# Performance work log

Measured on AMD Instinct MI355X. Metric: run time of the kernel, lower is better.

Reference implementation:

```python
import jax, jax.numpy as jnp
import numpy as np

N = 50000   # num nodes
D = 64      # feature dim
E = 800000  # num edges (avg degree 16)


def setup_inputs() -> dict:
    key = jax.random.key(0)
    k1, k2, k3 = jax.random.split(key, 3)
    x = jax.random.normal(k1, (N, D), dtype=jnp.float32)
    edge_index = jax.random.randint(k2, (2, E), 0, N, dtype=jnp.int32)
    edge_weight = jax.random.uniform(k3, (E,), dtype=jnp.float32)
    return {"x": x, "edge_index": edge_index, "edge_weight": edge_weight}


def reference(x, edge_index, edge_weight):
    """Faithful translation of scatter_median (spmm with reduce='median'):
    per destination node, the (lower) median over its weighted incoming
    neighbor messages, computed independently per feature channel.
    Nodes with zero in-degree produce zeros (as in the torch code where
    h is initialized to zeros and degree-0 rows are skipped).
    """
    n, d = x.shape
    e = edge_index.shape[1]

    # sort edges by destination (stable sort; within-segment order is irrelevant for median)
    order = jnp.argsort(edge_index[1])
    row = edge_index[0, order]
    col = edge_index[1, order]
    w = edge_weight[order]

    # weighted messages: x_j = x[row] * w  -> [E, D]
    x_j = x[row] * w[:, None]

    # per-destination degree and position of each edge within its segment
    deg = jnp.bincount(col, length=n)                                   # [N]
    starts = jnp.concatenate([jnp.zeros(1, deg.dtype), jnp.cumsum(deg)[:-1]])
    pos = jnp.arange(e, dtype=deg.dtype) - starts[col]                  # [E]

    # dense batch [N, max_deg, D], padded with +inf so pads sort to the end
    max_deg = int(jnp.max(deg))  # concrete on materialized inputs
    dense = jnp.full((n, max_deg, d), jnp.inf, dtype=x.dtype)
    dense = dense.at[col, pos].set(x_j)

    # per-channel sort, then pick the lower-median index (torch.median semantics:
    # for even counts it returns the lower of the two middle values)
    dense = jnp.sort(dense, axis=1)
    idx = jnp.maximum((deg - 1) // 2, 0)                                # [N]
    med = jnp.take_along_axis(dense, idx[:, None, None], axis=1)[:, 0]  # [N, D]

    return jnp.where(deg[:, None] > 0, med, jnp.zeros((), dtype=x.dtype))
```

## Files before the change

kernel.cpp:

```cpp
#include <hip/hip_runtime.h>
#include <stdint.h>
#include <math.h>

#define NN 50000
#define DD 64
#define EE 800000
#define CAP 64

__global__ void zero_deg(int* __restrict__ deg) {
    int i = blockIdx.x * blockDim.x + threadIdx.x;
    if (i < NN) deg[i] = 0;
}

__global__ __launch_bounds__(256) void scatter_edges(
        const int* __restrict__ ei, const float* __restrict__ ew,
        int* __restrict__ deg, uint64_t* __restrict__ slots) {
    int t = blockIdx.x * blockDim.x + threadIdx.x;
    int e0 = t * 2;
    if (e0 >= EE) return;

    int2   src2 = *reinterpret_cast<const int2*>(ei + e0);
    int2   dst2 = *reinterpret_cast<const int2*>(ei + EE + e0);
    float2 w2   = *reinterpret_cast<const float2*>(ew + e0);

    int p0 = atomicAdd(&deg[dst2.x], 1);
    int p1 = atomicAdd(&deg[dst2.y], 1);

    if (p0 < CAP) {
        uint64_t wb = (uint64_t)__float_as_uint(w2.x);
        slots[(size_t)dst2.x * CAP + p0] = (wb << 32) | (uint32_t)src2.x;
    }
    if (p1 < CAP) {
        uint64_t wb = (uint64_t)__float_as_uint(w2.y);
        slots[(size_t)dst2.y * CAP + p1] = (wb << 32) | (uint32_t)src2.y;
    }
}

__device__ __forceinline__ void cswap(float& a, float& b) {
    float lo = fminf(a, b);
    float hi = fmaxf(a, b);
    a = lo; b = hi;
}

template<int I, int END, int R, int STEP, int PW>
struct Pairs {
    static __device__ __forceinline__ void run(float (&r)[PW]) {
        if constexpr (I + R < END) {
            cswap(r[I], r[I + R]);
            Pairs<I + STEP, END, R, STEP, PW>::run(r);
        }
    }
};

template<int LO, int N, int R, int PW>
struct Merge {
    static __device__ __forceinline__ void run(float (&r)[PW]) {
        if constexpr (2 * R < N) {
            Merge<LO,     N, 2 * R, PW>::run(r);
            Merge<LO + R, N, 2 * R, PW>::run(r);
            Pairs<LO + R, LO + N, R, 2 * R, PW>::run(r);
        } else {
            cswap(r[LO], r[LO + R]);
        }
    }
};

template<int LO, int N, int PW>
struct Sorter {
    static __device__ __forceinline__ void run(float (&r)[PW]) {
        if constexpr (N > 1) {
            Sorter<LO,         N / 2, PW>::run(r);
            Sorter<LO + N / 2, N / 2, PW>::run(r);
            Merge<LO, N, 1, PW>::run(r);
        }
    }
};

template <int PW>
__device__ __forceinline__ float gather_sort(const float* __restrict__ x, int lane,
                                             int dg, int k, int src_l, float w_l) {
    float r[PW];
    #pragma unroll
    for (int j = 0; j < PW; ++j) {
        int   sj = __builtin_amdgcn_readlane(src_l, j);
        float wj = __uint_as_float((uint32_t)__builtin_amdgcn_readlane(
                       (int)__float_as_uint(w_l), j));
        float v = INFINITY;
        if (j < dg)
            v = x[(size_t)(uint32_t)sj * DD + lane] * wj;
        r[j] = v;
    }
    Sorter<0, PW, PW>::run(r);
    constexpr int KLO = PW / 4;
    constexpr int KHI = (PW / 2 > 0) ? PW / 2 - 1 : 0;
    float med = r[KLO];
    #pragma unroll
    for (int t = KLO + 1; t <= KHI; ++t)
        if (t == k) med = r[t];
    return med;
}

__global__ __launch_bounds__(256, 4) void median_kernel(
    const float* __restrict__ x, const int* __restrict__ deg,
    const uint64_t* __restrict__ slots, float* __restrict__ out) {
    const int lane = threadIdx.x & 63;
    const int n = blockIdx.x * 4 + (threadIdx.x >> 6);
    if (n >= NN) return;

    int dg = deg[n];
    if (dg > CAP) dg = CAP;
    if (dg == 0) { out[(size_t)n * DD + lane] = 0.f; return; }

    uint64_t s = 0;
    if (lane < dg) s = slots[(size_t)n * CAP + lane];
    int   src_l = (int)(uint32_t)(s & 0xffffffffu);
    float w_l   = __uint_as_float((uint32_t)(s >> 32));

    const int k = (dg - 1) >> 1;
    float med;

    if      (dg <= 2)  med = gather_sort<2>(x, lane, dg, k, src_l, w_l);
    else if (dg <= 4)  med = gather_sort<4>(x, lane, dg, k, src_l, w_l);
    else if (dg <= 8)  med = gather_sort<8>(x, lane, dg, k, src_l, w_l);
    else if (dg <= 16) med = gather_sort<16>(x, lane, dg, k, src_l, w_l);
    else if (dg <= 32) med = gather_sort<32>(x, lane, dg, k, src_l, w_l);
    else               med = gather_sort<64>(x, lane, dg, k, src_l, w_l);

    out[(size_t)n * DD + lane] = med;
}

extern "C" void kernel_launch(void* const* d_in, const int* in_sizes, int n_in,
                              void* d_out, int out_size, void* d_ws, size_t ws_size,
                              hipStream_t stream) {
    const float*  x  = (const float*)d_in[0];
    const int*    ei = (const int*)d_in[1];
    const float*  ew = (const float*)d_in[2];
    float* out = (float*)d_out;

    int*      deg   = (int*)d_ws;
    uint64_t* slots = (uint64_t*)((char*)d_ws + (1 << 18));

    zero_deg<<<(NN + 255) / 256, 256, 0, stream>>>(deg);
    scatter_edges<<<(EE / 2 + 255) / 256, 256, 0, stream>>>(ei, ew, deg, slots);
    median_kernel<<<(NN + 3) / 4, 256, 0, stream>>>(x, deg, slots, out);
}
```

Before: 162.3 us.

## Partition per-node degree counters by XCD to localize scatter atomics

Replaces the single global per-destination atomic counter with eight per-XCD counter arrays, each owning six slots per node. A shared overflow counter supplies sixteen extra slots per node. The change aims to keep most atomics local to one XCD's L2 by using workgroup-scope atomics on per-XCD arrays, avoiding cross-die coherence traffic. The median kernel compacts the scattered slots with a ballot/popcount prefix search and shuffles before the gather and sort. This adds more counter zeroing and reads, and relies on the XCC_ID register, workgroup-scope atomics being safe across workgroups on the same XCD, and degree per node staying within 64, with overflow capped at 16.

```diff
diff --git a/kernel.cpp b/kernel.cpp
--- a/kernel.cpp
+++ b/kernel.cpp
@@ -5,34 +5,48 @@
 #define NN 50000
 #define DD 64
 #define EE 800000
-#define CAP 64
+#define NXCD 8
+#define PCAP 6
+#define OCAP 16
 
-__global__ void zero_deg(int* __restrict__ deg) {
+
+__global__ void zero_cnt(int* __restrict__ cnt) {
     int i = blockIdx.x * blockDim.x + threadIdx.x;
-    if (i < NN) deg[i] = 0;
+    if (i < NN * (NXCD + 1)) cnt[i] = 0;
 }
 
 __global__ __launch_bounds__(256) void scatter_edges(
         const int* __restrict__ ei, const float* __restrict__ ew,
-        int* __restrict__ deg, uint64_t* __restrict__ slots) {
+        int* __restrict__ deg8, int* __restrict__ ovf,
+        uint64_t* __restrict__ slots) {
     int t = blockIdx.x * blockDim.x + threadIdx.x;
     int e0 = t * 2;
     if (e0 >= EE) return;
+
+    unsigned xcd;
+    asm volatile("s_getreg_b32 %0, hwreg(HW_REG_XCC_ID)" : "=s"(xcd));
+    xcd &= (NXCD - 1);
 
     int2   src2 = *reinterpret_cast<const int2*>(ei + e0);
     int2   dst2 = *reinterpret_cast<const int2*>(ei + EE + e0);
     float2 w2   = *reinterpret_cast<const float2*>(ew + e0);
 
-    int p0 = atomicAdd(&deg[dst2.x], 1);
-    int p1 = atomicAdd(&deg[dst2.y], 1);
+    int   d[2] = {dst2.x, dst2.y};
+    int   s[2] = {src2.x, src2.y};
+    float w[2] = {w2.x, w2.y};
 
-    if (p0 < CAP) {
-        uint64_t wb = (uint64_t)__float_as_uint(w2.x);
-        slots[(size_t)dst2.x * CAP + p0] = (wb << 32) | (uint32_t)src2.x;
-    }
-    if (p1 < CAP) {
-        uint64_t wb = (uint64_t)__float_as_uint(w2.y);
-        slots[(size_t)dst2.y * CAP + p1] = (wb << 32) | (uint32_t)src2.y;
+    #pragma unroll
+    for (int i = 0; i < 2; ++i) {
+        uint64_t pk = ((uint64_t)__float_as_uint(w[i]) << 32) | (uint32_t)s[i];
+        size_t base = (size_t)d[i] * 64;
+        int p = __hip_atomic_fetch_add(&deg8[xcd * NN + d[i]], 1,
+                                       __ATOMIC_RELAXED, __HIP_MEMORY_SCOPE_WORKGROUP);
+        if (p < PCAP) {
+            slots[base + xcd * PCAP + p] = pk;
+        } else {
+            int q = atomicAdd(&ovf[d[i]], 1);
+            if (q < OCAP) slots[base + 48 + q] = pk;
+        }
     }
 }
 
@@ -101,20 +115,42 @@
 }
 
 __global__ __launch_bounds__(256, 4) void median_kernel(
-    const float* __restrict__ x, const int* __restrict__ deg,
-    const uint64_t* __restrict__ slots, float* __restrict__ out) {
+    const float* __restrict__ x, const int* __restrict__ deg8,
+    const int* __restrict__ ovf, const uint64_t* __restrict__ slots,
+    float* __restrict__ out) {
     const int lane = threadIdx.x & 63;
     const int n = blockIdx.x * 4 + (threadIdx.x >> 6);
     if (n >= NN) return;
 
-    int dg = deg[n];
-    if (dg > CAP) dg = CAP;
+    int cnt, pos;
+    if (lane < 48) {
+        int xc = lane / 6;
+        pos = lane - xc * 6;
+        cnt = deg8[xc * NN + n];
+        if (cnt > PCAP) cnt = PCAP;
+    } else {
+        pos = lane - 48;
+        cnt = ovf[n];
+        if (cnt > OCAP) cnt = OCAP;
+    }
+    uint64_t mask = __ballot(pos < cnt);
+    int dg = __popcll(mask);
+
     if (dg == 0) { out[(size_t)n * DD + lane] = 0.f; return; }
 
-    uint64_t s = 0;
-    if (lane < dg) s = slots[(size_t)n * CAP + lane];
-    int   src_l = (int)(uint32_t)(s & 0xffffffffu);
-    float w_l   = __uint_as_float((uint32_t)(s >> 32));
+    uint64_t s = slots[(size_t)n * 64 + lane];
+    int   src_raw = (int)(uint32_t)(s & 0xffffffffu);
+    float w_raw   = __uint_as_float((uint32_t)(s >> 32));
+
+    int idx = 0;
+    #pragma unroll
+    for (int step = 32; step >= 1; step >>= 1) {
+        int t2 = idx + step;
+        uint64_t lowmask = (t2 >= 64) ? ~0ull : ((1ull << t2) - 1ull);
+        if (__popcll(mask & lowmask) <= lane) idx = t2;
+    }
+    int   src_l = __shfl(src_raw, idx);
+    float w_l   = __shfl(w_raw, idx);
 
     const int k = (dg - 1) >> 1;
     float med;
@@ -137,10 +173,11 @@
     const float*  ew = (const float*)d_in[2];
     float* out = (float*)d_out;
 
-    int*      deg   = (int*)d_ws;
-    uint64_t* slots = (uint64_t*)((char*)d_ws + (1 << 18));
+    int*      deg8  = (int*)d_ws;
+    int*      ovf   = (int*)((char*)d_ws + (size_t)NXCD * NN * 4);
+    uint64_t* slots = (uint64_t*)((char*)d_ws + (1u << 21));
 
-    zero_deg<<<(NN + 255) / 256, 256, 0, stream>>>(deg);
-    scatter_edges<<<(EE / 2 + 255) / 256, 256, 0, stream>>>(ei, ew, deg, slots);
-    median_kernel<<<(NN + 3) / 4, 256, 0, stream>>>(x, deg, slots, out);
+    zero_cnt<<<(NN * (NXCD + 1) + 255) / 256, 256, 0, stream>>>(deg8);
+    scatter_edges<<<(EE / 2 + 255) / 256, 256, 0, stream>>>(ei, ew, deg8, ovf, slots);
+    median_kernel<<<(NN + 3) / 4, 256, 0, stream>>>(x, deg8, ovf, slots, out);
 }
```

Result: slower. 175.4 us (+8.1%).

## Bucketize edges by 64-node groups with shared-memory histograms before median

Applied to the files above, without the earlier changes.

Replaces per-edge global atomics into per-node slots with a two-level bucketing scheme. Each block builds a shared-memory histogram over 64-node buckets and reserves space with one global atomic per bucket, then writes packed records. The median kernel loads one bucket per block and scatters its records into per-node slots in LDS using shared atomics. The aim is to cut global atomic contention and scattered writes. Buckets are capped at 1536 records, so an unusually dense bucket would drop edges, and the median kernel now launches only 782 blocks that each process 64 nodes serially per wave.

```diff
diff --git a/kernel.cpp b/kernel.cpp
--- a/kernel.cpp
+++ b/kernel.cpp
@@ -5,34 +5,52 @@
 #define NN 50000
 #define DD 64
 #define EE 800000
-#define CAP 64
+#define BSZ 64
+#define NB 782
+#define BCAP 1536
+#define EPW 4096
 
-__global__ void zero_deg(int* __restrict__ deg) {
+
+__global__ void zero_cnt(int* __restrict__ cnt) {
     int i = blockIdx.x * blockDim.x + threadIdx.x;
-    if (i < NN) deg[i] = 0;
+    if (i < NB) cnt[i] = 0;
 }
 
-__global__ __launch_bounds__(256) void scatter_edges(
+__global__ __launch_bounds__(256) void bucketize(
         const int* __restrict__ ei, const float* __restrict__ ew,
-        int* __restrict__ deg, uint64_t* __restrict__ slots) {
-    int t = blockIdx.x * blockDim.x + threadIdx.x;
-    int e0 = t * 2;
-    if (e0 >= EE) return;
+        int* __restrict__ bucket_cnt, uint64_t* __restrict__ recs) {
+    __shared__ int hist[NB];
+    __shared__ int base[NB];
+    const int t = threadIdx.x;
+    const int e0 = blockIdx.x * EPW;
+    const int eend = (e0 + EPW < EE) ? e0 + EPW : EE;
 
-    int2   src2 = *reinterpret_cast<const int2*>(ei + e0);
-    int2   dst2 = *reinterpret_cast<const int2*>(ei + EE + e0);
-    float2 w2   = *reinterpret_cast<const float2*>(ew + e0);
+    for (int i = t; i < NB; i += 256) hist[i] = 0;
+    __syncthreads();
 
-    int p0 = atomicAdd(&deg[dst2.x], 1);
-    int p1 = atomicAdd(&deg[dst2.y], 1);
+    for (int e = e0 + t; e < eend; e += 256) {
+        int dst = ei[EE + e];
+        atomicAdd(&hist[dst >> 6], 1);
+    }
+    __syncthreads();
 
-    if (p0 < CAP) {
-        uint64_t wb = (uint64_t)__float_as_uint(w2.x);
-        slots[(size_t)dst2.x * CAP + p0] = (wb << 32) | (uint32_t)src2.x;
+    for (int i = t; i < NB; i += 256) {
+        int c = hist[i];
+        base[i] = (c > 0) ? atomicAdd(&bucket_cnt[i], c) : 0;
+        hist[i] = 0;
     }
-    if (p1 < CAP) {
-        uint64_t wb = (uint64_t)__float_as_uint(w2.y);
-        slots[(size_t)dst2.y * CAP + p1] = (wb << 32) | (uint32_t)src2.y;
+    __syncthreads();
+
+    for (int e = e0 + t; e < eend; e += 256) {
+        int   src = ei[e];
+        int   dst = ei[EE + e];
+        float w   = ew[e];
+        int   b   = dst >> 6;
+        int   p   = base[b] + atomicAdd(&hist[b], 1);
+        if (p < BCAP)
+            recs[(size_t)b * BCAP + p] =
+                ((uint64_t)__float_as_uint(w) << 32) |
+                ((uint32_t)src << 6) | (uint32_t)(dst & 63);
     }
 }
 
@@ -100,33 +118,56 @@
     return med;
 }
 
-__global__ __launch_bounds__(256, 4) void median_kernel(
-    const float* __restrict__ x, const int* __restrict__ deg,
-    const uint64_t* __restrict__ slots, float* __restrict__ out) {
-    const int lane = threadIdx.x & 63;
-    const int n = blockIdx.x * 4 + (threadIdx.x >> 6);
-    if (n >= NN) return;
+__global__ __launch_bounds__(256) void median_kernel(
+    const float* __restrict__ x, const int* __restrict__ bucket_cnt,
+    const uint64_t* __restrict__ recs, float* __restrict__ out) {
+    __shared__ uint64_t slot[BSZ * 64];
+    __shared__ int degl[BSZ];
+    const int t = threadIdx.x;
+    const int b = blockIdx.x;
 
-    int dg = deg[n];
-    if (dg > CAP) dg = CAP;
-    if (dg == 0) { out[(size_t)n * DD + lane] = 0.f; return; }
+    int cnt = bucket_cnt[b];
+    if (cnt > BCAP) cnt = BCAP;
 
-    uint64_t s = 0;
-    if (lane < dg) s = slots[(size_t)n * CAP + lane];
-    int   src_l = (int)(uint32_t)(s & 0xffffffffu);
-    float w_l   = __uint_as_float((uint32_t)(s >> 32));
+    for (int i = t; i < BSZ; i += 256) degl[i] = 0;
+    __syncthreads();
 
-    const int k = (dg - 1) >> 1;
-    float med;
+    const uint64_t* brec = recs + (size_t)b * BCAP;
+    for (int i = t; i < cnt; i += 256) {
+        uint64_t r = brec[i];
+        int loc = (int)(r & 63u);
+        int p = atomicAdd(&degl[loc], 1);
+        if (p < 64)
+            slot[loc * 64 + p] = (r & 0xFFFFFFFF00000000ull)
+                               | (uint32_t)(((uint32_t)r) >> 6);
+    }
+    __syncthreads();
 
-    if      (dg <= 2)  med = gather_sort<2>(x, lane, dg, k, src_l, w_l);
-    else if (dg <= 4)  med = gather_sort<4>(x, lane, dg, k, src_l, w_l);
-    else if (dg <= 8)  med = gather_sort<8>(x, lane, dg, k, src_l, w_l);
-    else if (dg <= 16) med = gather_sort<16>(x, lane, dg, k, src_l, w_l);
-    else if (dg <= 32) med = gather_sort<32>(x, lane, dg, k, src_l, w_l);
-    else               med = gather_sort<64>(x, lane, dg, k, src_l, w_l);
+    const int lane = t & 63;
+    const int wv   = t >> 6;
+    for (int loc = wv; loc < BSZ; loc += 4) {
+        int n = b * BSZ + loc;
+        if (n >= NN) break;
 
-    out[(size_t)n * DD + lane] = med;
+        int dg = __builtin_amdgcn_readfirstlane(degl[loc]);
+        if (dg > 64) dg = 64;
+
+        float med = 0.f;
+        if (dg > 0) {
+            uint64_t s = slot[loc * 64 + lane];
+            int   src_l = (int)(uint32_t)(s & 0xffffffffu);
+            float w_l   = __uint_as_float((uint32_t)(s >> 32));
+            const int k = (dg - 1) >> 1;
+
+            if      (dg <= 2)  med = gather_sort<2>(x, lane, dg, k, src_l, w_l);
+            else if (dg <= 4)  med = gather_sort<4>(x, lane, dg, k, src_l, w_l);
+            else if (dg <= 8)  med = gather_sort<8>(x, lane, dg, k, src_l, w_l);
+            else if (dg <= 16) med = gather_sort<16>(x, lane, dg, k, src_l, w_l);
+            else if (dg <= 32) med = gather_sort<32>(x, lane, dg, k, src_l, w_l);
+            else               med = gather_sort<64>(x, lane, dg, k, src_l, w_l);
+        }
+        out[(size_t)n * DD + lane] = med;
+    }
 }
 
 extern "C" void kernel_launch(void* const* d_in, const int* in_sizes, int n_in,
@@ -137,10 +178,10 @@
     const float*  ew = (const float*)d_in[2];
     float* out = (float*)d_out;
 
-    int*      deg   = (int*)d_ws;
-    uint64_t* slots = (uint64_t*)((char*)d_ws + (1 << 18));
+    int*      bucket_cnt = (int*)d_ws;
+    uint64_t* recs       = (uint64_t*)((char*)d_ws + (1 << 16));
 
-    zero_deg<<<(NN + 255) / 256, 256, 0, stream>>>(deg);
-    scatter_edges<<<(EE / 2 + 255) / 256, 256, 0, stream>>>(ei, ew, deg, slots);
-    median_kernel<<<(NN + 3) / 4, 256, 0, stream>>>(x, deg, slots, out);
+    zero_cnt<<<(NB + 255) / 256, 256, 0, stream>>>(bucket_cnt);
+    bucketize<<<(EE + EPW - 1) / EPW, 256, 0, stream>>>(ei, ew, bucket_cnt, recs);
+    median_kernel<<<NB, 256, 0, stream>>>(x, bucket_cnt, recs, out);
 }
```

After: 148.4 us. 8.6% less time.
